# Kernel tuning notes

Measured on AMD Instinct MI355X. Metric: run time of the kernel, lower is better.

## Reference

```python
import jax, jax.numpy as jnp
import numpy as np

N = 50000
IN_CH = 128
OUT_CH = 64
H1, C1 = 8, 8


def gat_layer(x, src, dst, W, att_src, att_dst, bias, heads, out_ch, concat, n_nodes):
    # x: [N, F_in]; W: [F_in, heads*out_ch]; att_*: [heads, out_ch]; bias: [heads*out_ch] or [out_ch]
    h = (x @ W).reshape(n_nodes, heads, out_ch)              # [N,H,C]
    a_src = jnp.einsum('nhc,hc->nh', h, att_src)             # [N,H]
    a_dst = jnp.einsum('nhc,hc->nh', h, att_dst)             # [N,H]
    e = jax.nn.leaky_relu(a_src[src] + a_dst[dst], 0.2)      # [E,H]
    # segment softmax over incoming edges of each dst node
    m = jax.ops.segment_max(e, dst, num_segments=n_nodes)    # [N,H]
    p = jnp.exp(e - m[dst])                                  # [E,H]
    s = jax.ops.segment_sum(p, dst, num_segments=n_nodes)    # [N,H]
    alpha = p / (s[dst] + 1e-16)                             # [E,H]
    out = jax.ops.segment_sum(h[src] * alpha[:, :, None], dst, num_segments=n_nodes)  # [N,H,C]
    out = out.reshape(n_nodes, heads * out_ch) if concat else out.mean(axis=1)
    return out + bias


def setup_inputs() -> dict:
    key = jax.random.key(0)
    ks = jax.random.split(key, 12)
    E = 1600000
    x = jax.random.normal(ks[0], (N, IN_CH), dtype=jnp.float32)
    edge_index = jax.random.randint(ks[1], (2, E), 0, N, dtype=jnp.int64)
    sc = 0.1
    return {
        'x': x,
        'edge_index': edge_index,
        'W1': jax.random.normal(ks[2], (IN_CH, H1 * C1), dtype=jnp.float32) * sc,
        'att_src1': jax.random.normal(ks[3], (H1, C1), dtype=jnp.float32) * sc,
        'att_dst1': jax.random.normal(ks[4], (H1, C1), dtype=jnp.float32) * sc,
        'b1': jnp.zeros((H1 * C1,), dtype=jnp.float32),
        'W2': jax.random.normal(ks[5], (H1 * C1, OUT_CH), dtype=jnp.float32) * sc,
        'att_src2': jax.random.normal(ks[6], (1, OUT_CH), dtype=jnp.float32) * sc,
        'att_dst2': jax.random.normal(ks[7], (1, OUT_CH), dtype=jnp.float32) * sc,
        'b2': jnp.zeros((OUT_CH,), dtype=jnp.float32),
        'lin_W': jax.random.normal(ks[8], (OUT_CH, 1), dtype=jnp.float32) * sc,
        'lin_b': jnp.zeros((1,), dtype=jnp.float32),
    }


def reference(x, edge_index, W1, att_src1, att_dst1, b1, W2, att_src2, att_dst2, b2, lin_W, lin_b):
    # add self loops (PyG GATConv default)
    loops = jnp.arange(N, dtype=edge_index.dtype)
    src = jnp.concatenate([edge_index[0], loops])
    dst = jnp.concatenate([edge_index[1], loops])
    # dropout layers are identity in eval mode
    h = gat_layer(x, src, dst, W1, att_src1, att_dst1, b1, H1, C1, True, N)
    h = jax.nn.elu(h)
    h = gat_layer(h, src, dst, W2, att_src2, att_dst2, b2, 1, OUT_CH, False, N)
    return h @ lin_W + lin_b
```

## Files before the change

kernel.cpp:

```cpp
#include <hip/hip_runtime.h>
#include <hip/hip_bf16.h>
#include <math.h>

#define NN     50000
#define FIN    128
#define F1     64
#define NH1    8
#define F2     64

#define BSH    256
#define NB     ((NN + BSH - 1) / BSH)
#define BCAP   9472
#define PREB   13
#define MG1B   ((NN + 255) / 256)

typedef __bf16 bf16x8 __attribute__((ext_vector_type(8)));
typedef float  f32x4  __attribute__((ext_vector_type(4)));


__device__ __forceinline__ float loadF(const void* p, long long i, int fp32) {
    if (fp32) return ((const float*)p)[i];
    return __bfloat162float(((const __hip_bfloat16*)p)[i]);
}
__device__ __forceinline__ int loadI_nt(const void* p, long long i, int i64) {
    if (i64) return (int)__builtin_nontemporal_load(&((const long long*)p)[i]);
    return __builtin_nontemporal_load(&((const int*)p)[i]);
}
__device__ __forceinline__ unsigned short f2bfu(float f) {
    unsigned u = __float_as_uint(f);
    return (unsigned short)((u + 0x7FFFu + ((u >> 16) & 1u)) >> 16);
}
__device__ __forceinline__ float b2f(unsigned short u) {
    return __uint_as_float(((unsigned)u) << 16);
}


__global__ __launch_bounds__(1024) void k_front(
    const void* __restrict__ x, const void* __restrict__ ei, int E, int Etot,
    int* __restrict__ flags,
    const void* __restrict__ W1, const void* __restrict__ W2,
    unsigned short* __restrict__ W1p, unsigned short* __restrict__ W2p,
    int* __restrict__ bcnt, unsigned* __restrict__ binned) {
    __shared__ int s_a, s_b;
    __shared__ int hist[NB], gbase[NB];
    int tid = threadIdx.x;
    if (blockIdx.x < PREB) {
        if (tid == 0) { s_a = 0; s_b = 0; }
        __syncthreads();
        const unsigned short* u = (const unsigned short*)x;
        int cnt = 0;
        for (int i = tid; i < 8192; i += 1024) {
            unsigned short v = u[i];
            if ((v & 0x7F80) == 0x7F80) cnt++;
        }
        if (cnt) atomicAdd(&s_a, cnt);
        const unsigned* e32 = (const unsigned*)ei;
        int nz = 0;
        for (int i = tid; i < 2048; i += 1024) {
            if (e32[2 * i + 1] != 0u) nz++;
        }
        if (nz) atomicAdd(&s_b, nz);
        __syncthreads();
        int fp32 = (s_a > 2) ? 1 : 0;
        if (tid == 0 && blockIdx.x == 0) {
            flags[0] = fp32;
            flags[1] = (s_b == 0) ? 1 : 0;
        }
        int gt = blockIdx.x * 1024 + tid, gs = PREB * 1024;
        for (int i = gt; i < (FIN / 32) * 4 * 512; i += gs) {
            int j = i & 7, l = (i >> 3) & 63, f = i >> 9;
            int kb = f >> 2, nt = f & 3;
            int k = kb * 32 + (l >> 4) * 8 + j, n = nt * 16 + (l & 15);
            W1p[i] = f2bfu(loadF(W1, k * 64 + n, fp32));
        }
        for (int i = gt; i < (F1 / 32) * 4 * 512; i += gs) {
            int j = i & 7, l = (i >> 3) & 63, f = i >> 9;
            int kb = f >> 2, nt = f & 3;
            int k = kb * 32 + (l >> 4) * 8 + j, n = nt * 16 + (l & 15);
            W2p[i] = f2bfu(loadF(W2, k * 64 + n, fp32));
        }
    } else {
        if (tid == 0) s_b = 0;
        for (int i = tid; i < NB; i += 1024) hist[i] = 0;
        __syncthreads();
        const unsigned* e32 = (const unsigned*)ei;
        int nz = 0;
        for (int i = tid; i < 2048; i += 1024) {
            if (e32[2 * i + 1] != 0u) nz++;
        }
        if (nz) atomicAdd(&s_b, nz);
        __syncthreads();
        int i64 = (s_b == 0) ? 1 : 0;
        long long base = (long long)(blockIdx.x - PREB) * 8192;
        unsigned pk[8]; short bb[8];
        #pragma unroll
        for (int u = 0; u < 8; ++u) {
            long long j = base + u * 1024 + tid;
            int s = -1, d = -1;
            if (j < Etot) {
                if (j < E) { s = loadI_nt(ei, j, i64); d = loadI_nt(ei, (long long)E + j, i64); }
                else       { s = d = (int)(j - E); }
            }
            if ((unsigned)s < NN && (unsigned)d < NN) {
                bb[u] = (short)(d >> 8);
                pk[u] = ((unsigned)s << 8) | (unsigned)(d & 255);
                atomicAdd(&hist[bb[u]], 1);
            } else bb[u] = -1;
        }
        __syncthreads();
        for (int i = tid; i < NB; i += 1024) {
            int h = hist[i];
            gbase[i] = h ? atomicAdd(&bcnt[i], h) : 0;
            hist[i] = 0;
        }
        __syncthreads();
        #pragma unroll
        for (int u = 0; u < 8; ++u) {
            if (bb[u] >= 0) {
                int pos = gbase[bb[u]] + atomicAdd(&hist[bb[u]], 1);
                if (pos < BCAP) binned[(size_t)bb[u] * BCAP + pos] = pk[u];
            }
        }
    }
}


__global__ __launch_bounds__(1024) void k_mid(
    const int* __restrict__ bcnt, const unsigned* __restrict__ binned,
    int* __restrict__ offs, int* __restrict__ perm,
    const void* __restrict__ x, const unsigned short* __restrict__ W1p,
    const void* __restrict__ attS, const void* __restrict__ attD,
    __hip_bfloat16* __restrict__ h1, float* __restrict__ a1s,
    float* __restrict__ a1d, const int* __restrict__ flags) {
    __shared__ __align__(16) char smem[33280];
    int tid = threadIdx.x;
    if (blockIdx.x < NB) {
        int* hist = (int*)smem;
        int* cur  = (int*)(smem + 1024);
        int* sd   = (int*)(smem + 2048);
        int bk = blockIdx.x;
        int n0 = bk * BSH;
        if (tid < 256) sd[tid] = (tid < NB) ? min(bcnt[tid], BCAP) : 0;
        __syncthreads();
        for (int off = 1; off < BSH; off <<= 1) {
            int t = 0;
            if (tid < 256 && tid >= off) t = sd[tid - off];
            __syncthreads();
            if (tid < 256) sd[tid] += t;
            __syncthreads();
        }
        int gb = (bk > 0) ? sd[bk - 1] : 0;
        if (bk == 0 && tid == 0) offs[NN] = sd[NB - 1];
        __syncthreads();
        int cnt = bcnt[bk]; if (cnt > BCAP) cnt = BCAP;
        const unsigned* bp = binned + (size_t)bk * BCAP;
        if (tid < 256) hist[tid] = 0;
        __syncthreads();
        for (int i = tid; i < cnt; i += 1024)
            atomicAdd(&hist[bp[i] & 255], 1);
        __syncthreads();
        int myh = (tid < 256) ? hist[tid] : 0;
        if (tid < 256) sd[tid] = myh;
        __syncthreads();
        for (int off = 1; off < BSH; off <<= 1) {
            int t = 0;
            if (tid < 256 && tid >= off) t = sd[tid - off];
            __syncthreads();
            if (tid < 256) sd[tid] += t;
            __syncthreads();
        }
        if (tid < 256) {
            int excl = sd[tid] - myh;
            cur[tid] = gb + excl;
            if (n0 + tid < NN) offs[n0 + tid] = gb + excl;
        }
        __syncthreads();
        for (int i = tid; i < cnt; i += 1024) {
            unsigned pk = bp[i];
            int pos = atomicAdd(&cur[pk & 255], 1);
            perm[pos] = (int)(pk >> 8);
        }
    } else {
        int fp32 = flags[0];
        unsigned short* hl = (unsigned short*)smem;
        float* attSl = (float*)(smem + 32768);
        float* attDl = (float*)(smem + 32768 + 256);
        if (tid < 64) { attSl[tid] = loadF(attS, tid, fp32); attDl[tid] = loadF(attD, tid, fp32); }
        int sub = tid >> 8, t = tid & 255;
        int w = t >> 6, l = t & 63;
        int quad = l >> 4, lm = l & 15;
        int n0 = (blockIdx.x - NB) * 256 + sub * 64;
        unsigned short* hls = hl + sub * 4096;

        bf16x8 bfr[16];
        #pragma unroll
        for (int f = 0; f < 16; ++f)
            bfr[f] = *(const bf16x8*)(W1p + f * 512 + l * 8);

        int nodeA = n0 + w * 16 + lm;
        long long rowA = (nodeA < NN) ? nodeA : 0;
        f32x4 acc[4];
        #pragma unroll
        for (int nt = 0; nt < 4; ++nt) acc[nt] = (f32x4){0.f, 0.f, 0.f, 0.f};

        #pragma unroll
        for (int kb = 0; kb < 4; ++kb) {
            bf16x8 af;
            if (!fp32) {
                af = *(const bf16x8*)((const unsigned short*)x + rowA * FIN + kb * 32 + quad * 8);
            } else {
                const float* xf = (const float*)x + rowA * FIN + kb * 32 + quad * 8;
                union { unsigned short s[8]; bf16x8 v; } tmp;
                #pragma unroll
                for (int j = 0; j < 8; ++j) tmp.s[j] = f2bfu(xf[j]);
                af = tmp.v;
            }
            #pragma unroll
            for (int nt = 0; nt < 4; ++nt)
                acc[nt] = __builtin_amdgcn_mfma_f32_16x16x32_bf16(af, bfr[kb * 4 + nt], acc[nt], 0, 0, 0);
        }

        #pragma unroll
        for (int nt = 0; nt < 4; ++nt) {
            #pragma unroll
            for (int r = 0; r < 4; ++r) {
                int nl = w * 16 + quad * 4 + r;
                int node = n0 + nl;
                int c = nt * 16 + lm;
                unsigned short hb = f2bfu(acc[nt][r]);
                hls[nl * 64 + c] = hb;
                if (node < NN) ((unsigned short*)h1)[(size_t)node * 64 + c] = hb;
            }
        }
        __syncthreads();
        #pragma unroll
        for (int pp = 0; pp < 2; ++pp) {
            int p = t + pp * 256;
            int nl = p >> 3, g = p & 7;
            int node = n0 + nl;
            float ss = 0.f, dd = 0.f;
            #pragma unroll
            for (int j = 0; j < 8; ++j) {
                float hv = b2f(hls[nl * 64 + g * 8 + j]);
                ss += hv * attSl[g * 8 + j];
                dd += hv * attDl[g * 8 + j];
            }
            if (node < NN) {
                a1s[(size_t)node * NH1 + g] = ss;
                a1d[(size_t)node * NH1 + g] = dd;
            }
        }
    }
}


#define HLP 72

__global__ __launch_bounds__(256) void k_agg1f(
    const int* __restrict__ offs, const int* __restrict__ perm,
    const __hip_bfloat16* __restrict__ h1, const float* __restrict__ a1s,
    const float* __restrict__ a1d, const void* __restrict__ b1,
    const unsigned short* __restrict__ W2p,
    const void* __restrict__ attS2, const void* __restrict__ attD2,
    __hip_bfloat16* __restrict__ h2, float* __restrict__ a2s,
    float* __restrict__ a2d, int n, const int* __restrict__ flags) {
    int fp32 = flags[0];
    __shared__ unsigned short hl[16 * HLP];
    __shared__ float attSl[64], attDl[64];
    __shared__ float sp[16 * 4], dp[16 * 4];
    int tid = threadIdx.x;
    if (tid < 64) { attSl[tid] = loadF(attS2, tid, fp32); attDl[tid] = loadF(attD2, tid, fp32); }
    int w = tid >> 6, c = tid & 63;
    int n0 = blockIdx.x * 16;
    int u = c & 7, h = c >> 3, cb = c & 56;
    const unsigned short* hu = (const unsigned short*)h1;

    for (int m = 0; m < 4; ++m) {
        int d = n0 + w * 4 + m;
        if (d < n) {
            int start = offs[d], end = offs[d + 1];
            float adl = a1d[(size_t)d * NH1 + h];
            float acc = 0.f, denp = 0.f;
            for (int i = start; i < end; i += 8) {
                int j = i + u;
                int jc = (j < end) ? j : (end - 1);
                int sj = perm[jc];
                float e = a1s[(size_t)sj * NH1 + h] + adl;
                e = fmaxf(e, 0.2f * e);
                float p = (j < end) ? __expf(e) : 0.f;
                denp += p;
                #pragma unroll
                for (int k = 0; k < 8; ++k) {
                    int su = __builtin_amdgcn_readlane(sj, k);
                    float pk = __shfl(p, cb + k, 64);
                    acc = fmaf(pk, b2f(hu[(size_t)su * 64 + c]), acc);
                }
            }
            denp += __shfl_xor(denp, 1, 64);
            denp += __shfl_xor(denp, 2, 64);
            denp += __shfl_xor(denp, 4, 64);
            float v = acc / (denp + 1e-16f) + loadF(b1, c, fp32);
            v = (v > 0.f) ? v : expm1f(v);
            hl[(w * 4 + m) * HLP + c] = f2bfu(v);
        }
    }
    __syncthreads();

    int quad = c >> 4, lm = c & 15;
    bf16x8 bf0 = *(const bf16x8*)(W2p + (0 * 4 + w) * 512 + c * 8);
    bf16x8 bf1 = *(const bf16x8*)(W2p + (1 * 4 + w) * 512 + c * 8);
    bf16x8 af0 = *(const bf16x8*)(hl + lm * HLP + 0 * 32 + quad * 8);
    bf16x8 af1 = *(const bf16x8*)(hl + lm * HLP + 1 * 32 + quad * 8);
    f32x4 acc2 = (f32x4){0.f, 0.f, 0.f, 0.f};
    acc2 = __builtin_amdgcn_mfma_f32_16x16x32_bf16(af0, bf0, acc2, 0, 0, 0);
    acc2 = __builtin_amdgcn_mfma_f32_16x16x32_bf16(af1, bf1, acc2, 0, 0, 0);

    int cg = w * 16 + lm;
    float aSc = attSl[cg], aDc = attDl[cg];
    #pragma unroll
    for (int r = 0; r < 4; ++r) {
        int nl = quad * 4 + r;
        int node = n0 + nl;
        unsigned short hb = f2bfu(acc2[r]);
        if (node < n) ((unsigned short*)h2)[(size_t)node * 64 + cg] = hb;
        float hv = b2f(hb);
        float pvs = hv * aSc, pvd = hv * aDc;
        pvs += __shfl_xor(pvs, 1, 64); pvd += __shfl_xor(pvd, 1, 64);
        pvs += __shfl_xor(pvs, 2, 64); pvd += __shfl_xor(pvd, 2, 64);
        pvs += __shfl_xor(pvs, 4, 64); pvd += __shfl_xor(pvd, 4, 64);
        pvs += __shfl_xor(pvs, 8, 64); pvd += __shfl_xor(pvd, 8, 64);
        if (lm == 0) { sp[nl * 4 + w] = pvs; dp[nl * 4 + w] = pvd; }
    }
    __syncthreads();
    if (tid < 16) {
        int node = n0 + tid;
        if (node < n) {
            a2s[node] = sp[tid * 4 + 0] + sp[tid * 4 + 1] + sp[tid * 4 + 2] + sp[tid * 4 + 3];
            a2d[node] = dp[tid * 4 + 0] + dp[tid * 4 + 1] + dp[tid * 4 + 2] + dp[tid * 4 + 3];
        }
    }
}


__global__ __launch_bounds__(256) void k_agg2(
    const int* __restrict__ offs, const int* __restrict__ perm,
    const __hip_bfloat16* __restrict__ h2, const float* __restrict__ a2s,
    const float* __restrict__ a2d, const void* __restrict__ b2,
    const void* __restrict__ linW, const void* __restrict__ linb,
    void* __restrict__ out, int n, const int* __restrict__ flags) {
    int fp32 = flags[0];
    int w = threadIdx.x >> 6, c = threadIdx.x & 63;
    int d = blockIdx.x * 4 + w;
    if (d >= n) return;
    int start = offs[d], end = offs[d + 1];
    int u = c & 7;
    float ad = a2d[d];
    const unsigned short* hu = (const unsigned short*)h2;
    float acc = 0.f, denp = 0.f;
    for (int i = start; i < end; i += 8) {
        int j = i + u;
        int jc = (j < end) ? j : (end - 1);
        int sj = perm[jc];
        float e = a2s[sj] + ad;
        e = fmaxf(e, 0.2f * e);
        float p = (j < end) ? __expf(e) : 0.f;
        denp += (c < 8) ? p : 0.f;
        #pragma unroll
        for (int k = 0; k < 8; ++k) {
            int su = __builtin_amdgcn_readlane(sj, k);
            float pk = __uint_as_float(__builtin_amdgcn_readlane(__float_as_uint(p), k));
            acc = fmaf(pk, b2f(hu[(size_t)su * 64 + c]), acc);
        }
    }
    #pragma unroll
    for (int off = 1; off < 64; off <<= 1) denp += __shfl_xor(denp, off, 64);
    float v = acc / (denp + 1e-16f) + loadF(b2, c, fp32);
    float part = v * loadF(linW, c, fp32);
    #pragma unroll
    for (int off = 1; off < 64; off <<= 1) part += __shfl_xor(part, off, 64);
    if (c == 0) {
        float r = part + loadF(linb, 0, fp32);
        if (fp32) ((float*)out)[d] = r;
        else      ((__hip_bfloat16*)out)[d] = __float2bfloat16(r);
    }
}


static inline char* carve(char*& p, size_t bytes) {
    char* r = p;
    p += (bytes + 255) & ~size_t(255);
    return r;
}

extern "C" void kernel_launch(void* const* d_in, const int* in_sizes, int n_in,
                              void* d_out, int out_size, void* d_ws, size_t ws_size,
                              hipStream_t stream) {
    const void* x     = d_in[0];
    const void* ei    = d_in[1];
    const void* W1    = d_in[2];
    const void* attS1 = d_in[3];
    const void* attD1 = d_in[4];
    const void* b1    = d_in[5];
    const void* W2    = d_in[6];
    const void* attS2 = d_in[7];
    const void* attD2 = d_in[8];
    const void* b2    = d_in[9];
    const void* linW  = d_in[10];
    const void* linb  = d_in[11];

    int E    = in_sizes[1] / 2;
    int Etot = E + NN;

    char* p = (char*)d_ws;
    int*   flags = (int*)carve(p, 256);
    int*   bcnt  = (int*)carve(p, (size_t)NB * 4);
    unsigned short* W1p = (unsigned short*)carve(p, 8192 * 2);
    unsigned short* W2p = (unsigned short*)carve(p, 4096 * 2);
    int*   offs  = (int*)carve(p, (size_t)(NN + 1) * 4);
    int*   perm  = (int*)carve(p, (size_t)Etot * 4);
    unsigned* binned = (unsigned*)carve(p, (size_t)NB * BCAP * 4);
    float*    a1s    = (float*)carve(p, (size_t)NN * NH1 * 4);
    float*    a1d    = (float*)carve(p, (size_t)NN * NH1 * 4);
    __hip_bfloat16* h1 = (__hip_bfloat16*)carve(p, (size_t)NN * F1 * 2);
    __hip_bfloat16* h2 = (__hip_bfloat16*)carve(p, (size_t)NN * F2 * 2);
    float* a2s = (float*)carve(p, (size_t)NN * 4);
    float* a2d = (float*)carve(p, (size_t)NN * 4);

    hipMemsetAsync(bcnt, 0, (size_t)NB * 4, stream);

    int nbin = (Etot + 8191) / 8192;
    k_front<<<PREB + nbin, 1024, 0, stream>>>(x, ei, E, Etot, flags,
                                              W1, W2, W1p, W2p, bcnt, binned);
    k_mid<<<NB + MG1B, 1024, 0, stream>>>(bcnt, binned, offs, perm,
                                          x, W1p, attS1, attD1, h1, a1s, a1d, flags);
    k_agg1f<<<(NN + 15) / 16, 256, 0, stream>>>(offs, perm, h1, a1s, a1d, b1,
                                                W2p, attS2, attD2, h2, a2s, a2d, NN, flags);
    k_agg2<<<(NN + 3) / 4, 256, 0, stream>>>(offs, perm, h2, a2s, a2d, b2, linW, linb, d_out, NN, flags);
}
```

Baseline: 225.0 us.

## Fold final linear projection into layer-2 aggregation to aggregate scalars

Because layer 2 has one head and is followed by a linear map to a scalar, the projection h2·linW is computed per node in the layer-1 aggregation kernel and stored with a2s as a float2. The layer-2 aggregation then gathers one scalar per edge instead of a 64-wide bf16 row, and bias times linW is added as a constant. This removes the 128-byte-per-edge gather and the h2 buffer. Rounding changes slightly, since the projection now uses bf16-rounded h values before aggregation instead of after.

```diff
diff --git a/kernel.cpp b/kernel.cpp
--- a/kernel.cpp
+++ b/kernel.cpp
@@ -262,12 +262,13 @@
     const float* __restrict__ a1d, const void* __restrict__ b1,
     const unsigned short* __restrict__ W2p,
     const void* __restrict__ attS2, const void* __restrict__ attD2,
-    __hip_bfloat16* __restrict__ h2, float* __restrict__ a2s,
-    float* __restrict__ a2d, int n, const int* __restrict__ flags) {
+    const void* __restrict__ linW,
+    float2* __restrict__ g2s, float* __restrict__ a2d,
+    int n, const int* __restrict__ flags) {
     int fp32 = flags[0];
     __shared__ unsigned short hl[16 * HLP];
     __shared__ float attSl[64], attDl[64];
-    __shared__ float sp[16 * 4], dp[16 * 4];
+    __shared__ float sp[16 * 4], dp[16 * 4], gp[16 * 4];
     int tid = threadIdx.x;
     if (tid < 64) { attSl[tid] = loadF(attS2, tid, fp32); attDl[tid] = loadF(attD2, tid, fp32); }
     int w = tid >> 6, c = tid & 63;
@@ -317,26 +318,28 @@
 
     int cg = w * 16 + lm;
     float aSc = attSl[cg], aDc = attDl[cg];
+    float lWc = loadF(linW, cg, fp32);
     #pragma unroll
     for (int r = 0; r < 4; ++r) {
         int nl = quad * 4 + r;
-        int node = n0 + nl;
         unsigned short hb = f2bfu(acc2[r]);
-        if (node < n) ((unsigned short*)h2)[(size_t)node * 64 + cg] = hb;
         float hv = b2f(hb);
-        float pvs = hv * aSc, pvd = hv * aDc;
-        pvs += __shfl_xor(pvs, 1, 64); pvd += __shfl_xor(pvd, 1, 64);
-        pvs += __shfl_xor(pvs, 2, 64); pvd += __shfl_xor(pvd, 2, 64);
-        pvs += __shfl_xor(pvs, 4, 64); pvd += __shfl_xor(pvd, 4, 64);
-        pvs += __shfl_xor(pvs, 8, 64); pvd += __shfl_xor(pvd, 8, 64);
-        if (lm == 0) { sp[nl * 4 + w] = pvs; dp[nl * 4 + w] = pvd; }
+        float pvs = hv * aSc, pvd = hv * aDc, pvg = hv * lWc;
+        pvs += __shfl_xor(pvs, 1, 64); pvd += __shfl_xor(pvd, 1, 64); pvg += __shfl_xor(pvg, 1, 64);
+        pvs += __shfl_xor(pvs, 2, 64); pvd += __shfl_xor(pvd, 2, 64); pvg += __shfl_xor(pvg, 2, 64);
+        pvs += __shfl_xor(pvs, 4, 64); pvd += __shfl_xor(pvd, 4, 64); pvg += __shfl_xor(pvg, 4, 64);
+        pvs += __shfl_xor(pvs, 8, 64); pvd += __shfl_xor(pvd, 8, 64); pvg += __shfl_xor(pvg, 8, 64);
+        if (lm == 0) { sp[nl * 4 + w] = pvs; dp[nl * 4 + w] = pvd; gp[nl * 4 + w] = pvg; }
     }
     __syncthreads();
     if (tid < 16) {
         int node = n0 + tid;
         if (node < n) {
-            a2s[node] = sp[tid * 4 + 0] + sp[tid * 4 + 1] + sp[tid * 4 + 2] + sp[tid * 4 + 3];
-            a2d[node] = dp[tid * 4 + 0] + dp[tid * 4 + 1] + dp[tid * 4 + 2] + dp[tid * 4 + 3];
+            float ss = sp[tid * 4 + 0] + sp[tid * 4 + 1] + sp[tid * 4 + 2] + sp[tid * 4 + 3];
+            float dd = dp[tid * 4 + 0] + dp[tid * 4 + 1] + dp[tid * 4 + 2] + dp[tid * 4 + 3];
+            float gg = gp[tid * 4 + 0] + gp[tid * 4 + 1] + gp[tid * 4 + 2] + gp[tid * 4 + 3];
+            g2s[node] = make_float2(ss, gg);
+            a2d[node] = dd;
         }
     }
 }
@@ -344,42 +347,35 @@
 
 __global__ __launch_bounds__(256) void k_agg2(
     const int* __restrict__ offs, const int* __restrict__ perm,
-    const __hip_bfloat16* __restrict__ h2, const float* __restrict__ a2s,
-    const float* __restrict__ a2d, const void* __restrict__ b2,
-    const void* __restrict__ linW, const void* __restrict__ linb,
+    const float2* __restrict__ g2s, const float* __restrict__ a2d,
+    const void* __restrict__ b2, const void* __restrict__ linW,
+    const void* __restrict__ linb,
     void* __restrict__ out, int n, const int* __restrict__ flags) {
     int fp32 = flags[0];
     int w = threadIdx.x >> 6, c = threadIdx.x & 63;
     int d = blockIdx.x * 4 + w;
     if (d >= n) return;
     int start = offs[d], end = offs[d + 1];
-    int u = c & 7;
     float ad = a2d[d];
-    const unsigned short* hu = (const unsigned short*)h2;
-    float acc = 0.f, denp = 0.f;
-    for (int i = start; i < end; i += 8) {
-        int j = i + u;
-        int jc = (j < end) ? j : (end - 1);
-        int sj = perm[jc];
-        float e = a2s[sj] + ad;
+    float acc = 0.f, den = 0.f;
+    for (int i = start + c; i < end; i += 64) {
+        int s = perm[i];
+        float2 ag = g2s[s];
+        float e = ag.x + ad;
         e = fmaxf(e, 0.2f * e);
-        float p = (j < end) ? __expf(e) : 0.f;
-        denp += (c < 8) ? p : 0.f;
-        #pragma unroll
-        for (int k = 0; k < 8; ++k) {
-            int su = __builtin_amdgcn_readlane(sj, k);
-            float pk = __uint_as_float(__builtin_amdgcn_readlane(__float_as_uint(p), k));
-            acc = fmaf(pk, b2f(hu[(size_t)su * 64 + c]), acc);
-        }
-    }
+        float p = __expf(e);
+        acc = fmaf(p, ag.y, acc);
+        den += p;
+    }
+    float cst = loadF(b2, c, fp32) * loadF(linW, c, fp32);
     #pragma unroll
-    for (int off = 1; off < 64; off <<= 1) denp += __shfl_xor(denp, off, 64);
-    float v = acc / (denp + 1e-16f) + loadF(b2, c, fp32);
-    float part = v * loadF(linW, c, fp32);
-    #pragma unroll
-    for (int off = 1; off < 64; off <<= 1) part += __shfl_xor(part, off, 64);
+    for (int off = 1; off < 64; off <<= 1) {
+        acc += __shfl_xor(acc, off, 64);
+        den += __shfl_xor(den, off, 64);
+        cst += __shfl_xor(cst, off, 64);
+    }
     if (c == 0) {
-        float r = part + loadF(linb, 0, fp32);
+        float r = acc / (den + 1e-16f) + cst + loadF(linb, 0, fp32);
         if (fp32) ((float*)out)[d] = r;
         else      ((__hip_bfloat16*)out)[d] = __float2bfloat16(r);
     }
@@ -422,9 +418,8 @@
     float*    a1s    = (float*)carve(p, (size_t)NN * NH1 * 4);
     float*    a1d    = (float*)carve(p, (size_t)NN * NH1 * 4);
     __hip_bfloat16* h1 = (__hip_bfloat16*)carve(p, (size_t)NN * F1 * 2);
-    __hip_bfloat16* h2 = (__hip_bfloat16*)carve(p, (size_t)NN * F2 * 2);
-    float* a2s = (float*)carve(p, (size_t)NN * 4);
-    float* a2d = (float*)carve(p, (size_t)NN * 4);
+    float2* g2s = (float2*)carve(p, (size_t)NN * 8);
+    float*  a2d = (float*)carve(p, (size_t)NN * 4);
 
     hipMemsetAsync(bcnt, 0, (size_t)NB * 4, stream);
 
@@ -434,6 +429,6 @@
     k_mid<<<NB + MG1B, 1024, 0, stream>>>(bcnt, binned, offs, perm,
                                           x, W1p, attS1, attD1, h1, a1s, a1d, flags);
     k_agg1f<<<(NN + 15) / 16, 256, 0, stream>>>(offs, perm, h1, a1s, a1d, b1,
-                                                W2p, attS2, attD2, h2, a2s, a2d, NN, flags);
-    k_agg2<<<(NN + 3) / 4, 256, 0, stream>>>(offs, perm, h2, a2s, a2d, b2, linW, linb, d_out, NN, flags);
-}
+                                                W2p, attS2, attD2, linW, g2s, a2d, NN, flags);
+    k_agg2<<<(NN + 3) / 4, 256, 0, stream>>>(offs, perm, g2s, a2d, b2, linW, linb, d_out, NN, flags);
+}
```

Measured after the change: 203.0 us. 1.11x faster.
